# Kernel tuning notes

Measured on AMD Instinct MI355X. Metric: run time of the kernel, lower is better.

## Reference

```python
import jax, jax.numpy as jnp
import numpy as np

D_MODEL = 1024
N_HEADS = 16
D_K = D_MODEL // N_HEADS
D_FF = 4096
EPS = 1e-6


def setup_inputs() -> dict:
    key = jax.random.key(0)
    ks = jax.random.split(key, 12)
    s = 1.0 / np.sqrt(D_MODEL)
    inp = {
        "x": jax.random.normal(ks[0], (4, 2048, D_MODEL), jnp.float32),
        "src_mask": jnp.ones((4, 1, 1, 2048), jnp.int32),
        "Wq": jax.random.normal(ks[1], (D_MODEL, D_MODEL), jnp.float32) * s,
        "bq": jnp.zeros((D_MODEL,), jnp.float32),
        "Wk": jax.random.normal(ks[2], (D_MODEL, D_MODEL), jnp.float32) * s,
        "bk": jnp.zeros((D_MODEL,), jnp.float32),
        "Wv": jax.random.normal(ks[3], (D_MODEL, D_MODEL), jnp.float32) * s,
        "bv": jnp.zeros((D_MODEL,), jnp.float32),
        "Wo": jax.random.normal(ks[4], (D_MODEL, D_MODEL), jnp.float32) * s,
        "bo": jnp.zeros((D_MODEL,), jnp.float32),
        "W1": jax.random.normal(ks[5], (D_MODEL, D_FF), jnp.float32) * s,
        "b1": jnp.zeros((D_FF,), jnp.float32),
        "W2": jax.random.normal(ks[6], (D_FF, D_MODEL), jnp.float32) * (1.0 / np.sqrt(D_FF)),
        "b2": jnp.zeros((D_MODEL,), jnp.float32),
        # scalar LayerNormalization params (alpha=ones(1), bias=zeros(1)) for the 2 residual norms
        "ln1_alpha": jnp.ones((1,), jnp.float32),
        "ln1_bias": jnp.zeros((1,), jnp.float32),
        "ln2_alpha": jnp.ones((1,), jnp.float32),
        "ln2_bias": jnp.zeros((1,), jnp.float32),
    }
    return inp


def _layernorm(x, alpha, bias):
    # matches torch: mean + std (unbiased, ddof=1), (x-mean)/(std+eps)
    mean = jnp.mean(x, axis=-1, keepdims=True)
    std = jnp.std(x, axis=-1, keepdims=True, ddof=1)
    return alpha * ((x - mean) / (std + EPS)) + bias


def _mha(x, mask, Wq, bq, Wk, bk, Wv, bv, Wo, bo):
    B, S, _ = x.shape
    q = (x @ Wq + bq).reshape(B, S, N_HEADS, D_K).transpose(0, 2, 1, 3)
    k = (x @ Wk + bk).reshape(B, S, N_HEADS, D_K).transpose(0, 2, 1, 3)
    v = (x @ Wv + bv).reshape(B, S, N_HEADS, D_K).transpose(0, 2, 1, 3)
    scores = jnp.einsum("bhqd,bhkd->bhqk", q, k) / jnp.sqrt(jnp.float32(D_K))
    scores = jnp.where(mask == 0, jnp.float32(-1e9), scores)
    attn = jax.nn.softmax(scores, axis=-1)
    ctx = jnp.einsum("bhqk,bhkd->bhqd", attn, v)
    ctx = ctx.transpose(0, 2, 1, 3).reshape(B, S, D_MODEL)
    return ctx @ Wo + bo


def reference(x, src_mask, Wq, bq, Wk, bk, Wv, bv, Wo, bo, W1, b1, W2, b2,
              ln1_alpha, ln1_bias, ln2_alpha, ln2_bias):
    # pre-norm residual 1: self-attention
    h = _layernorm(x, ln1_alpha, ln1_bias)
    x = x + _mha(h, src_mask, Wq, bq, Wk, bk, Wv, bv, Wo, bo)
    # pre-norm residual 2: FFN
    h = _layernorm(x, ln2_alpha, ln2_bias)
    ff = jax.nn.relu(h @ W1 + b1) @ W2 + b2
    return x + ff
```

## Files before the change

kernel.cpp:

```cpp
#include <hip/hip_runtime.h>

typedef __attribute__((ext_vector_type(8))) short v8s;
typedef __attribute__((ext_vector_type(8))) unsigned short v8u;
typedef __attribute__((ext_vector_type(4))) unsigned short v4u;
typedef __attribute__((ext_vector_type(4))) float f32x4;

#define DEV __device__ __forceinline__

DEV unsigned short f2bf(float f) {
  union { float f; unsigned u; } v; v.f = f;
  unsigned r = v.u + 0x7fffu + ((v.u >> 16) & 1u);
  return (unsigned short)(r >> 16);
}

DEV float fexp2(float x) {
  float r; asm("v_exp_f32 %0, %1" : "=v"(r) : "v"(x)); return r;
}

DEV void gload16(const unsigned short* g, unsigned short* l) {
  __builtin_amdgcn_global_load_lds(
      (const __attribute__((address_space(1))) unsigned int*)g,
      (__attribute__((address_space(3))) unsigned int*)l, 16, 0, 0);
}

#define SL2E 0.1803368801111204f

__global__ __launch_bounds__(256) void ln_kernel(
    const float* __restrict__ x, unsigned short* __restrict__ h,
    const float* __restrict__ alpha, const float* __restrict__ beta)
{
  int row = blockIdx.x;
  int tid = threadIdx.x;
  const float4* xr = reinterpret_cast<const float4*>(x + (size_t)row * 1024);
  float4 v = xr[tid];
  float s  = v.x + v.y + v.z + v.w;
  float ss = v.x * v.x + v.y * v.y + v.z * v.z + v.w * v.w;
#pragma unroll
  for (int off = 1; off < 64; off <<= 1) {
    s  += __shfl_xor(s, off);
    ss += __shfl_xor(ss, off);
  }
  __shared__ float ps[4][2];
  int wid = tid >> 6, lane = tid & 63;
  if (lane == 0) { ps[wid][0] = s; ps[wid][1] = ss; }
  __syncthreads();
  s  = ps[0][0] + ps[1][0] + ps[2][0] + ps[3][0];
  ss = ps[0][1] + ps[1][1] + ps[2][1] + ps[3][1];
  float mean = s * (1.0f / 1024.0f);
  float var  = (ss - 1024.0f * mean * mean) * (1.0f / 1023.0f);
  float inv  = 1.0f / (sqrtf(fmaxf(var, 0.0f)) + 1e-6f);
  float a = alpha[0], b = beta[0];
  v4u o;
  o[0] = f2bf(a * ((v.x - mean) * inv) + b);
  o[1] = f2bf(a * ((v.y - mean) * inv) + b);
  o[2] = f2bf(a * ((v.z - mean) * inv) + b);
  o[3] = f2bf(a * ((v.w - mean) * inv) + b);
  *reinterpret_cast<v4u*>(h + (size_t)row * 1024 + tid * 4) = o;
}

__global__ __launch_bounds__(256) void transpose_convert(
    const float* __restrict__ W, unsigned short* __restrict__ Wt, int K, int N)
{
  __shared__ float t[32][33];
  int n0 = blockIdx.x * 32, k0 = blockIdx.y * 32;
  int tx = threadIdx.x, ty = threadIdx.y;
#pragma unroll
  for (int i = 0; i < 4; ++i)
    t[ty + i * 8][tx] = W[(size_t)(k0 + ty + i * 8) * N + n0 + tx];
  __syncthreads();
#pragma unroll
  for (int i = 0; i < 4; ++i)
    Wt[(size_t)(n0 + ty + i * 8) * K + k0 + tx] = f2bf(t[tx][ty + i * 8]);
}

enum { MODE_QKV = 0, MODE_RES = 2, MODE_FFN1 = 3 };

template <int MODE>
__global__ __launch_bounds__(512, 1) void gemm_256(
    const unsigned short* __restrict__ A, const unsigned short* __restrict__ Bt,
    const float* __restrict__ bias0, const float* __restrict__ bias1,
    const float* __restrict__ bias2,
    void* __restrict__ o0, void* __restrict__ o1, void* __restrict__ o2,
    int M, int N, int K)
{
  __shared__ unsigned short lds[2][512 * 64];

  int nbx = M >> 8, nwg = gridDim.x;
  int lin = blockIdx.x;
  int qq = nwg >> 3, rr = nwg & 7;
  int xcd = lin & 7, idx = lin >> 3;
  int swz = (xcd < rr ? xcd * (qq + 1) : rr * (qq + 1) + (xcd - rr) * qq) + idx;
  int bx = swz % nbx, by = swz / nbx;

  int tid = threadIdx.x, lane = tid & 63, wid = tid >> 6;
  int wm = wid >> 2, wn = wid & 3;
  int g = lane >> 4, c0 = lane & 15;
  int rowBase = bx * 256, colBase = by * 256;

  const unsigned short* Ab = A  + (size_t)rowBase * K;
  const unsigned short* Bb = Bt + (size_t)colBase * K;
  int NT = K >> 6;

  const unsigned short* src[8]; int dq[8];
#pragma unroll
  for (int i = 0; i < 8; ++i) {
    int q = i * 512 + tid;
    dq[i] = q;
    if (i < 4) {
      int r = q >> 3, p = q & 7;
      src[i] = Ab + (size_t)r * K + 8 * (p ^ (r & 7));
    } else {
      int qb2 = q - 2048, r = qb2 >> 3, p = qb2 & 7;
      src[i] = Bb + (size_t)r * K + 8 * (p ^ (r & 7));
    }
  }

  f32x4 acc[8][4];
#pragma unroll
  for (int m = 0; m < 8; ++m)
#pragma unroll
    for (int n = 0; n < 4; ++n) acc[m][n] = (f32x4){0.f, 0.f, 0.f, 0.f};

#define STG256(tt) do { \
    unsigned short* sb_ = &lds[(tt) & 1][0]; int ko_ = (tt) << 6; \
    _Pragma("unroll") for (int i = 0; i < 8; ++i) gload16(src[i] + ko_, sb_ + dq[i] * 8); \
  } while (0)

  STG256(0);
  asm volatile("s_waitcnt vmcnt(0)" ::: "memory");
  __builtin_amdgcn_s_barrier();
  asm volatile("" ::: "memory");

  for (int t = 0; t < NT; ++t) {
    const char* buf = (const char*)&lds[t & 1][0];
    bool more = (t + 1 < NT);
    if (more) STG256(t + 1);
    int e = (c0 & 7) << 4;

#pragma unroll
    for (int ph = 0; ph < 2; ++ph) {
      v8s af[8], bfr[4];
#pragma unroll
      for (int m = 0; m < 8; ++m) {
        int row = wm * 128 + m * 16 + c0;
        af[m] = *reinterpret_cast<const v8s*>(
            buf + row * 128 + ((ph * 64 + g * 16) ^ e));
      }
#pragma unroll
      for (int n = 0; n < 4; ++n) {
        int row = wn * 64 + n * 16 + c0;
        bfr[n] = *reinterpret_cast<const v8s*>(
            buf + 32768 + row * 128 + ((ph * 64 + g * 16) ^ e));
      }

      __builtin_amdgcn_s_setprio(1);
#pragma unroll
      for (int m = 0; m < 8; ++m)
#pragma unroll
        for (int n = 0; n < 4; ++n)
          acc[m][n] = __builtin_amdgcn_mfma_f32_16x16x32_bf16(
              af[m], bfr[n], acc[m][n], 0, 0, 0);
      __builtin_amdgcn_s_setprio(0);
    }

    if (more) asm volatile("s_waitcnt vmcnt(0)" ::: "memory");
    __builtin_amdgcn_sched_barrier(0);
    __builtin_amdgcn_s_barrier();
    asm volatile("" ::: "memory");
  }
#undef STG256

#pragma unroll
  for (int mf = 0; mf < 8; ++mf) {
#pragma unroll
    for (int nf = 0; nf < 4; ++nf) {
#pragma unroll
      for (int r = 0; r < 4; ++r) {
        int row = rowBase + wm * 128 + mf * 16 + g * 4 + r;
        int col = colBase + wn * 64 + nf * 16 + c0;
        float v = acc[mf][nf][r];
        if constexpr (MODE == MODE_QKV) {
          int sect = colBase >> 10;
          int cs = col & 1023;
          const float* bp = sect == 0 ? bias0 : (sect == 1 ? bias1 : bias2);
          v += bp[cs];
          int hh = cs >> 6, d = cs & 63;
          int b = row >> 11, sI = row & 2047;
          size_t bh = (size_t)(b * 16 + hh);
          if (sect == 0) {
            ((unsigned short*)o0)[(bh * 2048 + sI) * 64 + d] = f2bf(v * SL2E);
          } else if (sect == 1) {
            ((unsigned short*)o1)[(bh * 2048 + sI) * 64 + d] = f2bf(v);
          } else {
            int k6 = sI & 63;
            int slot = ((k6 >> 5) << 5) | (((k6 >> 2) & 3) << 3) |
                       (((k6 >> 4) & 1) << 2) | (k6 & 3);
            int e2 = slot ^ ((d & 7) << 3);
            ((unsigned short*)o2)[((bh * 32 + (sI >> 6)) * 64 + d) * 64 + e2] = f2bf(v);
          }
        } else {
          v += bias0[col];
          ((unsigned short*)o0)[(size_t)row * N + col] = f2bf(fmaxf(v, 0.0f));
        }
      }
    }
  }
}

#define BUF_ELEMS ((128 + 256) * 64)

DEV void stage_part(const unsigned short* Aptr, const unsigned short* Bptr,
                    unsigned short* buf, int K, int part, int wid, int lane)
{
  {
    int d = (part * 8 + wid) * 64 + lane;
    int r = d >> 3, p = d & 7;
    gload16(Aptr + (size_t)r * K + 8 * (p ^ (r & 7)),
            buf + (size_t)(part * 8 + wid) * 512);
  }
#pragma unroll
  for (int j = 0; j < 2; ++j) {
    int ib = part * 2 + j;
    int d = (ib * 8 + wid) * 64 + lane;
    int r = d >> 3, p = d & 7;
    gload16(Bptr + (size_t)r * K + 8 * (p ^ (r & 7)),
            buf + 128 * 64 + (size_t)(ib * 8 + wid) * 512);
  }
}

__global__ __launch_bounds__(512, 2) void gemm_pipe_res(
    const unsigned short* __restrict__ A, const unsigned short* __restrict__ Bt,
    const float* __restrict__ bias0, const float* __restrict__ resid,
    float* __restrict__ o0, int M, int N, int K)
{
  __shared__ unsigned short lds[3 * BUF_ELEMS];

  int nbx = M >> 7, nwg = gridDim.x;
  int lin = blockIdx.x;
  int qq = nwg >> 3, rr = nwg & 7;
  int xcd = lin & 7, idx = lin >> 3;
  int swz = (xcd < rr ? xcd * (qq + 1) : rr * (qq + 1) + (xcd - rr) * qq) + idx;
  int bx = swz % nbx, by = swz / nbx;

  int tid = threadIdx.x, lane = tid & 63, wid = tid >> 6;
  int wm = wid >> 2, wn = wid & 3;
  int g = lane >> 4, c0 = lane & 15;
  int rowBase = bx * 128, colBase = by * 256;

  const unsigned short* Ab = A  + (size_t)rowBase * K;
  const unsigned short* Bb = Bt + (size_t)colBase * K;
  int NT = K >> 6;

  f32x4 acc[4][4];
#pragma unroll
  for (int m = 0; m < 4; ++m)
#pragma unroll
    for (int n = 0; n < 4; ++n) acc[m][n] = (f32x4){0.f, 0.f, 0.f, 0.f};

  stage_part(Ab, Bb, lds, K, 0, wid, lane);
  stage_part(Ab, Bb, lds, K, 1, wid, lane);
  stage_part(Ab + 64, Bb + 64, lds + BUF_ELEMS, K, 0, wid, lane);
  stage_part(Ab + 64, Bb + 64, lds + BUF_ELEMS, K, 1, wid, lane);
  asm volatile("s_waitcnt vmcnt(6)" ::: "memory");
  __builtin_amdgcn_s_barrier();
  asm volatile("" ::: "memory");

  int cur = 0;
  for (int t = 0; t < NT; ++t) {
    const char* Abuf = (const char*)(lds + cur * BUF_ELEMS);
    const char* Bbuf = Abuf + 128 * 128;
    int nxt2 = cur + 2; if (nxt2 >= 3) nxt2 -= 3;
    unsigned short* sbuf = lds + nxt2 * BUF_ELEMS;
    bool doStage = (t + 2 < NT);
    int ks_ = (t + 2) << 6;
    int e = (c0 & 7) << 4;

#pragma unroll
    for (int ph = 0; ph < 2; ++ph) {
      v8s af[4], bfr[4];
#pragma unroll
      for (int m = 0; m < 4; ++m)
        af[m] = *reinterpret_cast<const v8s*>(
            Abuf + (wm * 64 + m * 16 + c0) * 128 + ((ph * 64 + g * 16) ^ e));
#pragma unroll
      for (int n = 0; n < 4; ++n)
        bfr[n] = *reinterpret_cast<const v8s*>(
            Bbuf + (wn * 64 + n * 16 + c0) * 128 + ((ph * 64 + g * 16) ^ e));

      if (doStage) stage_part(Ab + ks_, Bb + ks_, sbuf, K, ph, wid, lane);

      __builtin_amdgcn_s_setprio(1);
#pragma unroll
      for (int m = 0; m < 4; ++m)
#pragma unroll
        for (int n = 0; n < 4; ++n)
          acc[m][n] = __builtin_amdgcn_mfma_f32_16x16x32_bf16(
              af[m], bfr[n], acc[m][n], 0, 0, 0);
      __builtin_amdgcn_s_setprio(0);
    }

    if (doStage)            asm volatile("s_waitcnt vmcnt(6)" ::: "memory");
    else if (t + 1 < NT)    asm volatile("s_waitcnt vmcnt(0)" ::: "memory");
    __builtin_amdgcn_sched_barrier(0);
    __builtin_amdgcn_s_barrier();
    asm volatile("" ::: "memory");
    cur = cur + 1; if (cur >= 3) cur -= 3;
  }

#pragma unroll
  for (int mf = 0; mf < 4; ++mf) {
#pragma unroll
    for (int nf = 0; nf < 4; ++nf) {
#pragma unroll
      for (int r = 0; r < 4; ++r) {
        int row = rowBase + wm * 64 + mf * 16 + g * 4 + r;
        int col = colBase + wn * 64 + nf * 16 + c0;
        float v = acc[mf][nf][r] + bias0[col];
        o0[(size_t)row * N + col] = resid[(size_t)row * N + col] + v;
      }
    }
  }
}

__global__ __launch_bounds__(256) void attn_kernel(
    const unsigned short* __restrict__ q, const unsigned short* __restrict__ k,
    const unsigned short* __restrict__ vP, const int* __restrict__ mask,
    unsigned short* __restrict__ ctx)
{
  const int S = 2048, DK = 64, NT = 32;
  int bh = blockIdx.x;
  int b = bh >> 4, hh = bh & 15;
  int qbase = blockIdx.y * 128;
  int tid = threadIdx.x, lane = tid & 63, wid = tid >> 6;
  int g = lane >> 4, c0 = lane & 15;

  __shared__ unsigned short Ks[3 * 4096];
  __shared__ unsigned short Vs[3 * 4096];
  __shared__ unsigned short Mb[2048];

  const unsigned short* qb  = q  + (size_t)bh * S * DK;
  const unsigned short* kb  = k  + (size_t)bh * S * DK;
  const unsigned short* vPb = vP + (size_t)bh * 32 * 4096;
  const int* mb = mask + b * S;

  const int4* mb4 = reinterpret_cast<const int4*>(mb);
  int4 ma = mb4[tid * 2], mc = mb4[tid * 2 + 1];
  unsigned short bneg = f2bf(-1e9f);
  v8u bw;
  bw[0] = ma.x ? 0 : bneg; bw[1] = ma.y ? 0 : bneg;
  bw[2] = ma.z ? 0 : bneg; bw[3] = ma.w ? 0 : bneg;
  bw[4] = mc.x ? 0 : bneg; bw[5] = mc.y ? 0 : bneg;
  bw[6] = mc.z ? 0 : bneg; bw[7] = mc.w ? 0 : bneg;
  *reinterpret_cast<v8u*>(&Mb[tid * 8]) = bw;
  int ok = (ma.x && ma.y && ma.z && ma.w && mc.x && mc.y && mc.z && mc.w) ? 1 : 0;
  int allValid = __syncthreads_and(ok);

  int qrow = qbase + wid * 32 + c0;
  v8s aq[2][2];
#pragma unroll
  for (int s = 0; s < 2; ++s)
#pragma unroll
    for (int t = 0; t < 2; ++t)
      aq[s][t] = *reinterpret_cast<const v8s*>(
          &qb[(size_t)(qrow + s * 16) * DK + t * 32 + g * 8]);

  int i0 = tid, i1 = tid + 256;
  int r0 = i0 >> 3, m0 = i0 & 7;
  int r1 = i1 >> 3, m1 = i1 & 7;
  int ko0 = r0 * DK + 8 * (m0 ^ (r0 & 7));
  int ko1 = r1 * DK + 8 * (m1 ^ (r1 & 7));

  f32x4 acc[2][4];
#pragma unroll
  for (int s = 0; s < 2; ++s)
#pragma unroll
    for (int no = 0; no < 4; ++no) acc[s][no] = (f32x4){0.f, 0.f, 0.f, 0.f};
  float lsum0 = 0.f, lsum1 = 0.f;

#define ASTAGE(bi, tt) do { \
    int tb_ = (tt) * 4096; \
    gload16(kb + tb_ + ko0, Ks + (bi) * 4096 + i0 * 8); \
    gload16(kb + tb_ + ko1, Ks + (bi) * 4096 + i1 * 8); \
    gload16(vPb + tb_ + i0 * 8, Vs + (bi) * 4096 + i0 * 8); \
    gload16(vPb + tb_ + i1 * 8, Vs + (bi) * 4096 + i1 * 8); \
  } while (0)

  ASTAGE(0, 0);
  ASTAGE(1, 1);
  asm volatile("s_waitcnt vmcnt(4)" ::: "memory");
  __builtin_amdgcn_s_barrier();
  asm volatile("" ::: "memory");

  int cur = 0, nx2 = 2;
  for (int t = 0; t < NT; ++t) {
    bool more2 = (t + 2 < NT);
    if (more2) ASTAGE(nx2, t + 2);
    const unsigned short* Kc = Ks + cur * 4096;
    const unsigned short* Vc = Vs + cur * 4096;

    float p0[16], p1[16];
#pragma unroll
    for (int n = 0; n < 4; ++n) {
      int kvr = n * 16 + c0;
      const char* krow = (const char*)(Kc + kvr * DK);
      int sw = (kvr & 7) << 4;
      v8s ak0 = *reinterpret_cast<const v8s*>(krow + ((g * 16) ^ sw));
      v8s ak1 = *reinterpret_cast<const v8s*>(krow + ((64 + g * 16) ^ sw));
      f32x4 s0 = (f32x4){0.f, 0.f, 0.f, 0.f};
      f32x4 s1 = (f32x4){0.f, 0.f, 0.f, 0.f};
      s0 = __builtin_amdgcn_mfma_f32_16x16x32_bf16(ak0, aq[0][0], s0, 0, 0, 0);
      s0 = __builtin_amdgcn_mfma_f32_16x16x32_bf16(ak1, aq[0][1], s0, 0, 0, 0);
      s1 = __builtin_amdgcn_mfma_f32_16x16x32_bf16(ak0, aq[1][0], s1, 0, 0, 0);
      s1 = __builtin_amdgcn_mfma_f32_16x16x32_bf16(ak1, aq[1][1], s1, 0, 0, 0);
#pragma unroll
      for (int r = 0; r < 4; ++r) { p0[n * 4 + r] = s0[r]; p1[n * 4 + r] = s1[r]; }
    }
    if (!allValid) {
#pragma unroll
      for (int n = 0; n < 4; ++n) {
        v4u mbv = *reinterpret_cast<const v4u*>(&Mb[t * 64 + n * 16 + g * 4]);
#pragma unroll
        for (int r = 0; r < 4; ++r) {
          union { unsigned u; float f; } cv; cv.u = ((unsigned)mbv[r]) << 16;
          p0[n * 4 + r] += cv.f; p1[n * 4 + r] += cv.f;
        }
      }
    }

    float ts0 = 0.f, ts1 = 0.f;
#pragma unroll
    for (int i = 0; i < 16; ++i) {
      p0[i] = fexp2(p0[i]); ts0 += p0[i];
      p1[i] = fexp2(p1[i]); ts1 += p1[i];
    }
    lsum0 += ts0; lsum1 += ts1;

    v8s pb0[2], pb1[2];
#pragma unroll
    for (int c = 0; c < 2; ++c) {
      union { v8s s; unsigned u[4]; } k0, k1;
#pragma unroll
      for (int hp = 0; hp < 4; ++hp) {
        asm("v_cvt_pk_bf16_f32 %0, %1, %2"
            : "=v"(k0.u[hp]) : "v"(p0[c * 8 + 2 * hp]), "v"(p0[c * 8 + 2 * hp + 1]));
        asm("v_cvt_pk_bf16_f32 %0, %1, %2"
            : "=v"(k1.u[hp]) : "v"(p1[c * 8 + 2 * hp]), "v"(p1[c * 8 + 2 * hp + 1]));
      }
      pb0[c] = k0.s; pb1[c] = k1.s;
    }

#pragma unroll
    for (int c = 0; c < 2; ++c) {
#pragma unroll
      for (int no = 0; no < 4; ++no) {
        int d = no * 16 + c0;
        v8s av = *reinterpret_cast<const v8s*>(
            (const char*)(Vc + d * 64) + ((c * 64 + g * 16) ^ ((d & 7) << 4)));
        acc[0][no] = __builtin_amdgcn_mfma_f32_16x16x32_bf16(av, pb0[c], acc[0][no], 0, 0, 0);
        acc[1][no] = __builtin_amdgcn_mfma_f32_16x16x32_bf16(av, pb1[c], acc[1][no], 0, 0, 0);
      }
    }

    if (more2)              asm volatile("s_waitcnt vmcnt(4)" ::: "memory");
    else if (t + 1 < NT)    asm volatile("s_waitcnt vmcnt(0)" ::: "memory");
    __builtin_amdgcn_sched_barrier(0);
    __builtin_amdgcn_s_barrier();
    asm volatile("" ::: "memory");
    cur = (cur + 1 < 3) ? cur + 1 : 0;
    nx2 = (nx2 + 1 < 3) ? nx2 + 1 : 0;
  }
#undef ASTAGE

  lsum0 += __shfl_xor(lsum0, 16); lsum0 += __shfl_xor(lsum0, 32);
  lsum1 += __shfl_xor(lsum1, 16); lsum1 += __shfl_xor(lsum1, 32);
  float lrow[2] = {lsum0, lsum1};

#pragma unroll
  for (int s = 0; s < 2; ++s) {
    float inv = 1.0f / fmaxf(lrow[s], 1e-30f);
#pragma unroll
    for (int no = 0; no < 4; ++no) {
      v4u o;
      o[0] = f2bf(acc[s][no][0] * inv);
      o[1] = f2bf(acc[s][no][1] * inv);
      o[2] = f2bf(acc[s][no][2] * inv);
      o[3] = f2bf(acc[s][no][3] * inv);
      *reinterpret_cast<v4u*>(
          &ctx[(size_t)(b * S + qrow + s * 16) * 1024 + hh * 64 + no * 16 + g * 4]) = o;
    }
  }
}

extern "C" void kernel_launch(void* const* d_in, const int* in_sizes, int n_in,
                              void* d_out, int out_size, void* d_ws, size_t ws_size,
                              hipStream_t stream)
{
  (void)in_sizes; (void)n_in; (void)out_size; (void)ws_size;
  const float* x    = (const float*)d_in[0];
  const int*   mask = (const int*)d_in[1];
  const float* Wq = (const float*)d_in[2];  const float* bq = (const float*)d_in[3];
  const float* Wk = (const float*)d_in[4];  const float* bk = (const float*)d_in[5];
  const float* Wv = (const float*)d_in[6];  const float* bv = (const float*)d_in[7];
  const float* Wo = (const float*)d_in[8];  const float* bo = (const float*)d_in[9];
  const float* W1 = (const float*)d_in[10]; const float* b1 = (const float*)d_in[11];
  const float* W2 = (const float*)d_in[12]; const float* b2 = (const float*)d_in[13];
  const float* ln1a = (const float*)d_in[14]; const float* ln1b = (const float*)d_in[15];
  const float* ln2a = (const float*)d_in[16]; const float* ln2b = (const float*)d_in[17];

  char* ws = (char*)d_ws;
  const size_t MB = (size_t)1 << 20;
  unsigned short* wqkvT = (unsigned short*)(ws + 0 * MB);
  unsigned short* woT = (unsigned short*)(ws + 6 * MB);
  unsigned short* w1T = (unsigned short*)(ws + 8 * MB);
  unsigned short* w2T = (unsigned short*)(ws + 16 * MB);
  unsigned short* hb  = (unsigned short*)(ws + 24 * MB);
  unsigned short* qb  = (unsigned short*)(ws + 40 * MB);
  unsigned short* kb  = (unsigned short*)(ws + 56 * MB);
  unsigned short* vPb = (unsigned short*)(ws + 72 * MB);
  unsigned short* ctx = (unsigned short*)(ws + 88 * MB);
  unsigned short* gb  = (unsigned short*)(ws + 40 * MB);
  float* xout = (float*)d_out;

  dim3 tb(32, 8);
  transpose_convert<<<dim3(32, 32),  tb, 0, stream>>>(Wq, wqkvT,               1024, 1024);
  transpose_convert<<<dim3(32, 32),  tb, 0, stream>>>(Wk, wqkvT + 1024 * 1024, 1024, 1024);
  transpose_convert<<<dim3(32, 32),  tb, 0, stream>>>(Wv, wqkvT + 2048 * 1024, 1024, 1024);
  transpose_convert<<<dim3(32, 32),  tb, 0, stream>>>(Wo, woT, 1024, 1024);
  transpose_convert<<<dim3(128, 32), tb, 0, stream>>>(W1, w1T, 1024, 4096);
  transpose_convert<<<dim3(32, 128), tb, 0, stream>>>(W2, w2T, 4096, 1024);

  ln_kernel<<<8192, 256, 0, stream>>>(x, hb, ln1a, ln1b);

  gemm_256<MODE_QKV><<<384, 512, 0, stream>>>(
      hb, wqkvT, bq, bk, bv, qb, kb, vPb, 8192, 3072, 1024);

  attn_kernel<<<dim3(64, 16), 256, 0, stream>>>(qb, kb, vPb, mask, ctx);

  gemm_pipe_res<<<256, 512, 0, stream>>>(ctx, woT, bo, x, xout, 8192, 1024, 1024);

  ln_kernel<<<8192, 256, 0, stream>>>(xout, hb, ln2a, ln2b);

  gemm_256<MODE_FFN1><<<512, 512, 0, stream>>>(
      hb, w1T, b1, nullptr, nullptr, gb, nullptr, nullptr, 8192, 4096, 1024);

  gemm_pipe_res<<<256, 512, 0, stream>>>(gb, w2T, b2, xout, xout, 8192, 1024, 4096);
}
```

Measured before the change: 401.4 us.

## Retile QKV GEMM, split FFN1 staging, and widen attention query tile

The QKV projection moves from the 256x256 double-buffered GEMM to a 128x256 triple-buffered pipelined kernel with two blocks per CU and 768 workgroups. FFN1 staging is split across the two k-phases so prefetch interleaves with MFMA, and the LDS swizzle uses the row index directly. The attention kernel processes 64 query rows per wave (256 per block), which halves K/V loads per query. It also computes the softmax row sum with an MFMA against a ones vector instead of scalar adds and shuffles. The trade-offs are more register pressure in attention and fewer attention blocks.

After: 368.4 us. 1.09x faster.

```diff
diff --git a/kernel.cpp b/kernel.cpp
--- a/kernel.cpp
+++ b/kernel.cpp
@@ -73,14 +73,142 @@
     Wt[(size_t)(n0 + ty + i * 8) * K + k0 + tx] = f2bf(t[tx][ty + i * 8]);
 }
 
-enum { MODE_QKV = 0, MODE_RES = 2, MODE_FFN1 = 3 };
-
-template <int MODE>
-__global__ __launch_bounds__(512, 1) void gemm_256(
+#define BUF_ELEMS ((128 + 256) * 64)
+
+DEV void stage_part(const unsigned short* Aptr, const unsigned short* Bptr,
+                    unsigned short* buf, int K, int part, int wid, int lane)
+{
+  {
+    int d = (part * 8 + wid) * 64 + lane;
+    int r = d >> 3, p = d & 7;
+    gload16(Aptr + (size_t)r * K + 8 * (p ^ (r & 7)),
+            buf + (size_t)(part * 8 + wid) * 512);
+  }
+#pragma unroll
+  for (int j = 0; j < 2; ++j) {
+    int ib = part * 2 + j;
+    int d = (ib * 8 + wid) * 64 + lane;
+    int r = d >> 3, p = d & 7;
+    gload16(Bptr + (size_t)r * K + 8 * (p ^ (r & 7)),
+            buf + 128 * 64 + (size_t)(ib * 8 + wid) * 512);
+  }
+}
+
+__global__ __launch_bounds__(512, 2) void gemm_qkv(
     const unsigned short* __restrict__ A, const unsigned short* __restrict__ Bt,
-    const float* __restrict__ bias0, const float* __restrict__ bias1,
-    const float* __restrict__ bias2,
-    void* __restrict__ o0, void* __restrict__ o1, void* __restrict__ o2,
+    const float* __restrict__ bq, const float* __restrict__ bk2,
+    const float* __restrict__ bv,
+    unsigned short* __restrict__ oq, unsigned short* __restrict__ ok2,
+    unsigned short* __restrict__ ov, int M, int N, int K)
+{
+  __shared__ unsigned short lds[3 * BUF_ELEMS];
+
+  int nbx = M >> 7, nwg = gridDim.x;
+  int lin = blockIdx.x;
+  int qq = nwg >> 3, rr = nwg & 7;
+  int xcd = lin & 7, idx = lin >> 3;
+  int swz = (xcd < rr ? xcd * (qq + 1) : rr * (qq + 1) + (xcd - rr) * qq) + idx;
+  int bx = swz % nbx, by = swz / nbx;
+
+  int tid = threadIdx.x, lane = tid & 63, wid = tid >> 6;
+  int wm = wid >> 2, wn = wid & 3;
+  int g = lane >> 4, c0 = lane & 15;
+  int rowBase = bx * 128, colBase = by * 256;
+
+  const unsigned short* Ab = A  + (size_t)rowBase * K;
+  const unsigned short* Bb = Bt + (size_t)colBase * K;
+  int NT = K >> 6;
+
+  f32x4 acc[4][4];
+#pragma unroll
+  for (int m = 0; m < 4; ++m)
+#pragma unroll
+    for (int n = 0; n < 4; ++n) acc[m][n] = (f32x4){0.f, 0.f, 0.f, 0.f};
+
+  stage_part(Ab, Bb, lds, K, 0, wid, lane);
+  stage_part(Ab, Bb, lds, K, 1, wid, lane);
+  stage_part(Ab + 64, Bb + 64, lds + BUF_ELEMS, K, 0, wid, lane);
+  stage_part(Ab + 64, Bb + 64, lds + BUF_ELEMS, K, 1, wid, lane);
+  asm volatile("s_waitcnt vmcnt(6)" ::: "memory");
+  __builtin_amdgcn_s_barrier();
+  asm volatile("" ::: "memory");
+
+  int cur = 0;
+  for (int t = 0; t < NT; ++t) {
+    const char* Abuf = (const char*)(lds + cur * BUF_ELEMS);
+    const char* Bbuf = Abuf + 128 * 128;
+    int nxt2 = cur + 2; if (nxt2 >= 3) nxt2 -= 3;
+    unsigned short* sbuf = lds + nxt2 * BUF_ELEMS;
+    bool doStage = (t + 2 < NT);
+    int ks_ = (t + 2) << 6;
+    int e = (c0 & 7) << 4;
+
+#pragma unroll
+    for (int ph = 0; ph < 2; ++ph) {
+      v8s af[4], bfr[4];
+#pragma unroll
+      for (int m = 0; m < 4; ++m)
+        af[m] = *reinterpret_cast<const v8s*>(
+            Abuf + (wm * 64 + m * 16 + c0) * 128 + ((ph * 64 + g * 16) ^ e));
+#pragma unroll
+      for (int n = 0; n < 4; ++n)
+        bfr[n] = *reinterpret_cast<const v8s*>(
+            Bbuf + (wn * 64 + n * 16 + c0) * 128 + ((ph * 64 + g * 16) ^ e));
+
+      if (doStage) stage_part(Ab + ks_, Bb + ks_, sbuf, K, ph, wid, lane);
+
+      __builtin_amdgcn_s_setprio(1);
+#pragma unroll
+      for (int m = 0; m < 4; ++m)
+#pragma unroll
+        for (int n = 0; n < 4; ++n)
+          acc[m][n] = __builtin_amdgcn_mfma_f32_16x16x32_bf16(
+              af[m], bfr[n], acc[m][n], 0, 0, 0);
+      __builtin_amdgcn_s_setprio(0);
+    }
+
+    if (doStage)            asm volatile("s_waitcnt vmcnt(6)" ::: "memory");
+    else if (t + 1 < NT)    asm volatile("s_waitcnt vmcnt(0)" ::: "memory");
+    __builtin_amdgcn_sched_barrier(0);
+    __builtin_amdgcn_s_barrier();
+    asm volatile("" ::: "memory");
+    cur = cur + 1; if (cur >= 3) cur -= 3;
+  }
+
+#pragma unroll
+  for (int mf = 0; mf < 4; ++mf) {
+#pragma unroll
+    for (int nf = 0; nf < 4; ++nf) {
+#pragma unroll
+      for (int r = 0; r < 4; ++r) {
+        int row = rowBase + wm * 64 + mf * 16 + g * 4 + r;
+        int col = colBase + wn * 64 + nf * 16 + c0;
+        int sect = colBase >> 10;
+        int cs = col & 1023;
+        const float* bp = sect == 0 ? bq : (sect == 1 ? bk2 : bv);
+        float v = acc[mf][nf][r] + bp[cs];
+        int hh = cs >> 6, d = cs & 63;
+        int b = row >> 11, sI = row & 2047;
+        size_t bh = (size_t)(b * 16 + hh);
+        if (sect == 0) {
+          oq[(bh * 2048 + sI) * 64 + d] = f2bf(v * SL2E);
+        } else if (sect == 1) {
+          ok2[(bh * 2048 + sI) * 64 + d] = f2bf(v);
+        } else {
+          int k6 = sI & 63;
+          int slot = ((k6 >> 5) << 5) | (((k6 >> 2) & 3) << 3) |
+                     (((k6 >> 4) & 1) << 2) | (k6 & 3);
+          int e2 = slot ^ ((d & 7) << 3);
+          ov[((bh * 32 + (sI >> 6)) * 64 + d) * 64 + e2] = f2bf(v);
+        }
+      }
+    }
+  }
+}
+
+__global__ __launch_bounds__(512, 1) void gemm_ffn1_256(
+    const unsigned short* __restrict__ A, const unsigned short* __restrict__ Bt,
+    const float* __restrict__ bias, unsigned short* __restrict__ out,
     int M, int N, int K)
 {
   __shared__ unsigned short lds[2][512 * 64];
@@ -121,12 +249,12 @@
 #pragma unroll
     for (int n = 0; n < 4; ++n) acc[m][n] = (f32x4){0.f, 0.f, 0.f, 0.f};
 
-#define STG256(tt) do { \
+#define STG256(tt, lo, hi) do { \
     unsigned short* sb_ = &lds[(tt) & 1][0]; int ko_ = (tt) << 6; \
-    _Pragma("unroll") for (int i = 0; i < 8; ++i) gload16(src[i] + ko_, sb_ + dq[i] * 8); \
+    _Pragma("unroll") for (int i = lo; i < hi; ++i) gload16(src[i] + ko_, sb_ + dq[i] * 8); \
   } while (0)
 
-  STG256(0);
+  STG256(0, 0, 8);
   asm volatile("s_waitcnt vmcnt(0)" ::: "memory");
   __builtin_amdgcn_s_barrier();
   asm volatile("" ::: "memory");
@@ -134,7 +262,6 @@
   for (int t = 0; t < NT; ++t) {
     const char* buf = (const char*)&lds[t & 1][0];
     bool more = (t + 1 < NT);
-    if (more) STG256(t + 1);
     int e = (c0 & 7) << 4;
 
 #pragma unroll
@@ -144,14 +271,16 @@
       for (int m = 0; m < 8; ++m) {
         int row = wm * 128 + m * 16 + c0;
         af[m] = *reinterpret_cast<const v8s*>(
-            buf + row * 128 + ((ph * 64 + g * 16) ^ e));
+            buf + row * 128 + ((ph * 64 + g * 16) ^ ((row & 7) << 4)));
       }
 #pragma unroll
       for (int n = 0; n < 4; ++n) {
         int row = wn * 64 + n * 16 + c0;
         bfr[n] = *reinterpret_cast<const v8s*>(
-            buf + 32768 + row * 128 + ((ph * 64 + g * 16) ^ e));
-      }
+            buf + 32768 + row * 128 + ((ph * 64 + g * 16) ^ ((row & 7) << 4)));
+      }
+
+      if (more) { if (ph == 0) STG256(t + 1, 0, 4); else STG256(t + 1, 4, 8); }
 
       __builtin_amdgcn_s_setprio(1);
 #pragma unroll
@@ -178,53 +307,10 @@
       for (int r = 0; r < 4; ++r) {
         int row = rowBase + wm * 128 + mf * 16 + g * 4 + r;
         int col = colBase + wn * 64 + nf * 16 + c0;
-        float v = acc[mf][nf][r];
-        if constexpr (MODE == MODE_QKV) {
-          int sect = colBase >> 10;
-          int cs = col & 1023;
-          const float* bp = sect == 0 ? bias0 : (sect == 1 ? bias1 : bias2);
-          v += bp[cs];
-          int hh = cs >> 6, d = cs & 63;
-          int b = row >> 11, sI = row & 2047;
-          size_t bh = (size_t)(b * 16 + hh);
-          if (sect == 0) {
-            ((unsigned short*)o0)[(bh * 2048 + sI) * 64 + d] = f2bf(v * SL2E);
-          } else if (sect == 1) {
-            ((unsigned short*)o1)[(bh * 2048 + sI) * 64 + d] = f2bf(v);
-          } else {
-            int k6 = sI & 63;
-            int slot = ((k6 >> 5) << 5) | (((k6 >> 2) & 3) << 3) |
-                       (((k6 >> 4) & 1) << 2) | (k6 & 3);
-            int e2 = slot ^ ((d & 7) << 3);
-            ((unsigned short*)o2)[((bh * 32 + (sI >> 6)) * 64 + d) * 64 + e2] = f2bf(v);
-          }
-        } else {
-          v += bias0[col];
-          ((unsigned short*)o0)[(size_t)row * N + col] = f2bf(fmaxf(v, 0.0f));
-        }
-      }
-    }
-  }
-}
-
-#define BUF_ELEMS ((128 + 256) * 64)
-
-DEV void stage_part(const unsigned short* Aptr, const unsigned short* Bptr,
-                    unsigned short* buf, int K, int part, int wid, int lane)
-{
-  {
-    int d = (part * 8 + wid) * 64 + lane;
-    int r = d >> 3, p = d & 7;
-    gload16(Aptr + (size_t)r * K + 8 * (p ^ (r & 7)),
-            buf + (size_t)(part * 8 + wid) * 512);
-  }
-#pragma unroll
-  for (int j = 0; j < 2; ++j) {
-    int ib = part * 2 + j;
-    int d = (ib * 8 + wid) * 64 + lane;
-    int r = d >> 3, p = d & 7;
-    gload16(Bptr + (size_t)r * K + 8 * (p ^ (r & 7)),
-            buf + 128 * 64 + (size_t)(ib * 8 + wid) * 512);
+        float v = acc[mf][nf][r] + bias[col];
+        out[(size_t)row * N + col] = f2bf(fmaxf(v, 0.0f));
+      }
+    }
   }
 }
 
@@ -322,7 +408,7 @@
   }
 }
 
-__global__ __launch_bounds__(256) void attn_kernel(
+__global__ __launch_bounds__(256, 2) void attn_kernel(
     const unsigned short* __restrict__ q, const unsigned short* __restrict__ k,
     const unsigned short* __restrict__ vP, const int* __restrict__ mask,
     unsigned short* __restrict__ ctx)
@@ -330,7 +416,7 @@
   const int S = 2048, DK = 64, NT = 32;
   int bh = blockIdx.x;
   int b = bh >> 4, hh = bh & 15;
-  int qbase = blockIdx.y * 128;
+  int qbase = blockIdx.y * 256;
   int tid = threadIdx.x, lane = tid & 63, wid = tid >> 6;
   int g = lane >> 4, c0 = lane & 15;
 
@@ -352,13 +438,13 @@
   bw[4] = mc.x ? 0 : bneg; bw[5] = mc.y ? 0 : bneg;
   bw[6] = mc.z ? 0 : bneg; bw[7] = mc.w ? 0 : bneg;
   *reinterpret_cast<v8u*>(&Mb[tid * 8]) = bw;
-  int ok = (ma.x && ma.y && ma.z && ma.w && mc.x && mc.y && mc.z && mc.w) ? 1 : 0;
-  int allValid = __syncthreads_and(ok);
-
-  int qrow = qbase + wid * 32 + c0;
-  v8s aq[2][2];
-#pragma unroll
-  for (int s = 0; s < 2; ++s)
+  int okm = (ma.x && ma.y && ma.z && ma.w && mc.x && mc.y && mc.z && mc.w) ? 1 : 0;
+  int allValid = __syncthreads_and(okm);
+
+  int qrow = qbase + wid * 64 + c0;
+  v8s aq[4][2];
+#pragma unroll
+  for (int s = 0; s < 4; ++s)
 #pragma unroll
     for (int t = 0; t < 2; ++t)
       aq[s][t] = *reinterpret_cast<const v8s*>(
@@ -370,12 +456,16 @@
   int ko0 = r0 * DK + 8 * (m0 ^ (r0 & 7));
   int ko1 = r1 * DK + 8 * (m1 ^ (r1 & 7));
 
-  f32x4 acc[2][4];
-#pragma unroll
-  for (int s = 0; s < 2; ++s)
+  f32x4 acc[4][4], accl[4];
+#pragma unroll
+  for (int s = 0; s < 4; ++s) {
+    accl[s] = (f32x4){0.f, 0.f, 0.f, 0.f};
 #pragma unroll
     for (int no = 0; no < 4; ++no) acc[s][no] = (f32x4){0.f, 0.f, 0.f, 0.f};
-  float lsum0 = 0.f, lsum1 = 0.f;
+  }
+  v8s ones;
+#pragma unroll
+  for (int j = 0; j < 8; ++j) ones[j] = (short)0x3F80;
 
 #define ASTAGE(bi, tt) do { \
     int tb_ = (tt) * 4096; \
@@ -398,57 +488,54 @@
     const unsigned short* Kc = Ks + cur * 4096;
     const unsigned short* Vc = Vs + cur * 4096;
 
-    float p0[16], p1[16];
-#pragma unroll
-    for (int n = 0; n < 4; ++n) {
-      int kvr = n * 16 + c0;
-      const char* krow = (const char*)(Kc + kvr * DK);
-      int sw = (kvr & 7) << 4;
-      v8s ak0 = *reinterpret_cast<const v8s*>(krow + ((g * 16) ^ sw));
-      v8s ak1 = *reinterpret_cast<const v8s*>(krow + ((64 + g * 16) ^ sw));
-      f32x4 s0 = (f32x4){0.f, 0.f, 0.f, 0.f};
-      f32x4 s1 = (f32x4){0.f, 0.f, 0.f, 0.f};
-      s0 = __builtin_amdgcn_mfma_f32_16x16x32_bf16(ak0, aq[0][0], s0, 0, 0, 0);
-      s0 = __builtin_amdgcn_mfma_f32_16x16x32_bf16(ak1, aq[0][1], s0, 0, 0, 0);
-      s1 = __builtin_amdgcn_mfma_f32_16x16x32_bf16(ak0, aq[1][0], s1, 0, 0, 0);
-      s1 = __builtin_amdgcn_mfma_f32_16x16x32_bf16(ak1, aq[1][1], s1, 0, 0, 0);
-#pragma unroll
-      for (int r = 0; r < 4; ++r) { p0[n * 4 + r] = s0[r]; p1[n * 4 + r] = s1[r]; }
-    }
-    if (!allValid) {
+    v8s pb[4][2];
+#pragma unroll
+    for (int pp = 0; pp < 2; ++pp) {
+      float pA[16], pB[16];
 #pragma unroll
       for (int n = 0; n < 4; ++n) {
-        v4u mbv = *reinterpret_cast<const v4u*>(&Mb[t * 64 + n * 16 + g * 4]);
-#pragma unroll
-        for (int r = 0; r < 4; ++r) {
-          union { unsigned u; float f; } cv; cv.u = ((unsigned)mbv[r]) << 16;
-          p0[n * 4 + r] += cv.f; p1[n * 4 + r] += cv.f;
+        int kvr = n * 16 + c0;
+        const char* krow = (const char*)(Kc + kvr * DK);
+        int sw = (kvr & 7) << 4;
+        v8s ak0 = *reinterpret_cast<const v8s*>(krow + ((g * 16) ^ sw));
+        v8s ak1 = *reinterpret_cast<const v8s*>(krow + ((64 + g * 16) ^ sw));
+        f32x4 s0 = (f32x4){0.f, 0.f, 0.f, 0.f};
+        f32x4 s1 = (f32x4){0.f, 0.f, 0.f, 0.f};
+        s0 = __builtin_amdgcn_mfma_f32_16x16x32_bf16(ak0, aq[pp * 2][0], s0, 0, 0, 0);
+        s0 = __builtin_amdgcn_mfma_f32_16x16x32_bf16(ak1, aq[pp * 2][1], s0, 0, 0, 0);
+        s1 = __builtin_amdgcn_mfma_f32_16x16x32_bf16(ak0, aq[pp * 2 + 1][0], s1, 0, 0, 0);
+        s1 = __builtin_amdgcn_mfma_f32_16x16x32_bf16(ak1, aq[pp * 2 + 1][1], s1, 0, 0, 0);
+#pragma unroll
+        for (int r = 0; r < 4; ++r) { pA[n * 4 + r] = s0[r]; pB[n * 4 + r] = s1[r]; }
+      }
+      if (!allValid) {
+#pragma unroll
+        for (int n = 0; n < 4; ++n) {
+          v4u mbv = *reinterpret_cast<const v4u*>(&Mb[t * 64 + n * 16 + g * 4]);
+#pragma unroll
+          for (int r = 0; r < 4; ++r) {
+            union { unsigned u; float f; } cv; cv.u = ((unsigned)mbv[r]) << 16;
+            pA[n * 4 + r] += cv.f; pB[n * 4 + r] += cv.f;
+          }
         }
       }
-    }
-
-    float ts0 = 0.f, ts1 = 0.f;
-#pragma unroll
-    for (int i = 0; i < 16; ++i) {
-      p0[i] = fexp2(p0[i]); ts0 += p0[i];
-      p1[i] = fexp2(p1[i]); ts1 += p1[i];
-    }
-    lsum0 += ts0; lsum1 += ts1;
-
-    v8s pb0[2], pb1[2];
-#pragma unroll
-    for (int c = 0; c < 2; ++c) {
-      union { v8s s; unsigned u[4]; } k0, k1;
-#pragma unroll
-      for (int hp = 0; hp < 4; ++hp) {
-        asm("v_cvt_pk_bf16_f32 %0, %1, %2"
-            : "=v"(k0.u[hp]) : "v"(p0[c * 8 + 2 * hp]), "v"(p0[c * 8 + 2 * hp + 1]));
-        asm("v_cvt_pk_bf16_f32 %0, %1, %2"
-            : "=v"(k1.u[hp]) : "v"(p1[c * 8 + 2 * hp]), "v"(p1[c * 8 + 2 * hp + 1]));
-      }
-      pb0[c] = k0.s; pb1[c] = k1.s;
-    }
-
+#pragma unroll
+      for (int i = 0; i < 16; ++i) { pA[i] = fexp2(pA[i]); pB[i] = fexp2(pB[i]); }
+#pragma unroll
+      for (int c = 0; c < 2; ++c) {
+        union { v8s s; unsigned u[4]; } kA, kB;
+#pragma unroll
+        for (int hp = 0; hp < 4; ++hp) {
+          asm("v_cvt_pk_bf16_f32 %0, %1, %2"
+              : "=v"(kA.u[hp]) : "v"(pA[c * 8 + 2 * hp]), "v"(pA[c * 8 + 2 * hp + 1]));
+          asm("v_cvt_pk_bf16_f32 %0, %1, %2"
+              : "=v"(kB.u[hp]) : "v"(pB[c * 8 + 2 * hp]), "v"(pB[c * 8 + 2 * hp + 1]));
+        }
+        pb[pp * 2][c] = kA.s; pb[pp * 2 + 1][c] = kB.s;
+      }
+    }
+
+    __builtin_amdgcn_s_setprio(1);
 #pragma unroll
     for (int c = 0; c < 2; ++c) {
 #pragma unroll
@@ -456,10 +543,15 @@
         int d = no * 16 + c0;
         v8s av = *reinterpret_cast<const v8s*>(
             (const char*)(Vc + d * 64) + ((c * 64 + g * 16) ^ ((d & 7) << 4)));
-        acc[0][no] = __builtin_amdgcn_mfma_f32_16x16x32_bf16(av, pb0[c], acc[0][no], 0, 0, 0);
-        acc[1][no] = __builtin_amdgcn_mfma_f32_16x16x32_bf16(av, pb1[c], acc[1][no], 0, 0, 0);
-      }
-    }
+#pragma unroll
+        for (int s = 0; s < 4; ++s)
+          acc[s][no] = __builtin_amdgcn_mfma_f32_16x16x32_bf16(av, pb[s][c], acc[s][no], 0, 0, 0);
+      }
+#pragma unroll
+      for (int s = 0; s < 4; ++s)
+        accl[s] = __builtin_amdgcn_mfma_f32_16x16x32_bf16(ones, pb[s][c], accl[s], 0, 0, 0);
+    }
+    __builtin_amdgcn_s_setprio(0);
 
     if (more2)              asm volatile("s_waitcnt vmcnt(4)" ::: "memory");
     else if (t + 1 < NT)    asm volatile("s_waitcnt vmcnt(0)" ::: "memory");
@@ -471,13 +563,9 @@
   }
 #undef ASTAGE
 
-  lsum0 += __shfl_xor(lsum0, 16); lsum0 += __shfl_xor(lsum0, 32);
-  lsum1 += __shfl_xor(lsum1, 16); lsum1 += __shfl_xor(lsum1, 32);
-  float lrow[2] = {lsum0, lsum1};
-
-#pragma unroll
-  for (int s = 0; s < 2; ++s) {
-    float inv = 1.0f / fmaxf(lrow[s], 1e-30f);
+#pragma unroll
+  for (int s = 0; s < 4; ++s) {
+    float inv = 1.0f / fmaxf(accl[s][0], 1e-30f);
 #pragma unroll
     for (int no = 0; no < 4; ++no) {
       v4u o;
@@ -531,17 +619,15 @@
 
   ln_kernel<<<8192, 256, 0, stream>>>(x, hb, ln1a, ln1b);
 
-  gemm_256<MODE_QKV><<<384, 512, 0, stream>>>(
-      hb, wqkvT, bq, bk, bv, qb, kb, vPb, 8192, 3072, 1024);
-
-  attn_kernel<<<dim3(64, 16), 256, 0, stream>>>(qb, kb, vPb, mask, ctx);
+  gemm_qkv<<<768, 512, 0, stream>>>(hb, wqkvT, bq, bk, bv, qb, kb, vPb, 8192, 3072, 1024);
+
+  attn_kernel<<<dim3(64, 8), 256, 0, stream>>>(qb, kb, vPb, mask, ctx);
 
   gemm_pipe_res<<<256, 512, 0, stream>>>(ctx, woT, bo, x, xout, 8192, 1024, 1024);
 
   ln_kernel<<<8192, 256, 0, stream>>>(xout, hb, ln2a, ln2b);
 
-  gemm_256<MODE_FFN1><<<512, 512, 0, stream>>>(
-      hb, w1T, b1, nullptr, nullptr, gb, nullptr, nullptr, 8192, 4096, 1024);
+  gemm_ffn1_256<<<512, 512, 0, stream>>>(hb, w1T, b1, gb, 8192, 4096, 1024);
 
   gemm_pipe_res<<<256, 512, 0, stream>>>(gb, w2T, b2, xout, xout, 8192, 1024, 4096);
 }
```
